# Performance work log

Hardware: AMD Instinct MI355X
Metric: run time of the kernel (lower is better)

Reference implementation:

```python
import jax, jax.numpy as jnp
import numpy as np

SCALE_FACTORS = (1, 2, 4)
N, T, F = 4096, 128, 128
MARKET = 64
MIX = sum(T // k for k in SCALE_FACTORS)  # 224


def hardswish(x):
    return x * jnp.clip(x + 3.0, 0.0, 6.0) * (1.0 / 6.0)


def layernorm2d(x, g, b, eps=1e-5):
    # LayerNorm with normalized_shape == last two dims (as in torch nn.LayerNorm((A, B)))
    mu = jnp.mean(x, axis=(-2, -1), keepdims=True)
    var = jnp.var(x, axis=(-2, -1), keepdims=True)
    return (x - mu) * jax.lax.rsqrt(var + eps) * g + b


def setup_inputs() -> dict:
    key = jax.random.key(0)
    ks = jax.random.split(key, 32)
    inp = {"x": jax.random.normal(ks[0], (N, T, F), jnp.float32)}
    i = 1
    for si, k in enumerate(SCALE_FACTORS):
        tk = T // k
        inp[f"cw{si}"] = jax.random.normal(ks[i], (F, F, k), jnp.float32) * 0.05; i += 1
        inp[f"cb{si}"] = jnp.zeros((F,), jnp.float32)
        inp[f"lg{si}"] = jnp.ones((tk, F), jnp.float32)
        inp[f"lb{si}"] = jnp.zeros((tk, F), jnp.float32)
        inp[f"L1_{si}"] = jax.random.normal(ks[i], (tk, tk), jnp.float32) * 0.01; i += 1
        inp[f"L2_{si}"] = jax.random.normal(ks[i], (tk, tk), jnp.float32) * 0.01; i += 1
    inp["fc_w"] = jax.random.normal(ks[i], (1, F), jnp.float32) * 0.05; i += 1
    inp["fc_b"] = jnp.zeros((1,), jnp.float32)
    inp["sm_lg"] = jnp.ones((N, MIX), jnp.float32)
    inp["sm_lb"] = jnp.zeros((N, MIX), jnp.float32)
    inp["M1"] = jax.random.normal(ks[i], (MARKET, N), jnp.float32); i += 1
    inp["M2"] = jax.random.normal(ks[i], (N, MARKET), jnp.float32); i += 1
    inp["sm_fc_w"] = jax.random.normal(ks[i], (1, 2 * MIX), jnp.float32) * 0.02; i += 1
    inp["sm_fc_b"] = jnp.zeros((1,), jnp.float32)
    return inp


def _forward(x, cw0, cb0, lg0, lb0, L1_0, L2_0,
             cw1, cb1, lg1, lb1, L1_1, L2_1,
             cw2, cb2, lg2, lb2, L1_2, L2_2,
             fc_w, fc_b, sm_lg, sm_lb, M1, M2, sm_fc_w, sm_fc_b):
    n, t, f = x.shape
    per_scale = ((cw0, cb0, lg0, lb0, L1_0, L2_0),
                 (cw1, cb1, lg1, lb1, L1_1, L2_1),
                 (cw2, cb2, lg2, lb2, L1_2, L2_2))
    parts = []
    for k, (cw, cb, lg, lb, L1, L2) in zip(SCALE_FACTORS, per_scale):
        tk = t // k
        # Conv1d(kernel=k, stride=k) == blockwise contraction over non-overlapping windows
        xr = x.transpose(0, 2, 1).reshape(n, f, tk, k)          # (n, F_in, tk, k)
        xt = jnp.einsum('nitk,oik->nto', xr, cw) + cb            # (n, tk, F)
        # TimeMixing: ragged prefix loop == single lower-triangular matmul over time
        mask = jnp.tril(jnp.ones((tk, tk), x.dtype))
        h = layernorm2d(xt, lg, lb)
        u = hardswish(jnp.einsum('ts,nsf->ntf', L1 * mask, h))
        v = jnp.einsum('ts,nsf->ntf', L2 * mask, u)
        xt = xt + v
        parts.append(xt @ fc_w[0] + fc_b[0])                     # (n, tk)
    h = jnp.concatenate(parts, axis=1)                           # (n, MIX)
    # StockMixing
    hn = layernorm2d(h, sm_lg, sm_lb)
    z = M2 @ hardswish(M1 @ hn)                                  # (n, MIX)
    out = jnp.concatenate([h, h + z], axis=1)                    # (n, 2*MIX)
    return out @ sm_fc_w[0][:, None] + sm_fc_b                   # (n, 1)


def reference(x, cw0, cb0, lg0, lb0, L1_0, L2_0,
              cw1, cb1, lg1, lb1, L1_1, L2_1,
              cw2, cb2, lg2, lb2, L1_2, L2_2,
              fc_w, fc_b, sm_lg, sm_lb, M1, M2, sm_fc_w, sm_fc_b):
    return _forward(x, cw0, cb0, lg0, lb0, L1_0, L2_0,
                    cw1, cb1, lg1, lb1, L1_1, L2_1,
                    cw2, cb2, lg2, lb2, L1_2, L2_2,
                    fc_w, fc_b, sm_lg, sm_lb, M1, M2, sm_fc_w, sm_fc_b)
```

## Files before the change

### kernel.cpp

```cpp
#include <hip/hip_runtime.h>
#include <stdint.h>

typedef __attribute__((ext_vector_type(8))) short short8;
typedef __attribute__((ext_vector_type(4))) float f32x4;
typedef __attribute__((ext_vector_type(4))) unsigned short us4;

__device__ __forceinline__ unsigned short f2bf(float f) {
  union { float f; unsigned int i; } v; v.f = f;
  return (unsigned short)((v.i + 0x7FFFu + ((v.i >> 16) & 1u)) >> 16);
}
__device__ __forceinline__ float hswish(float x) {
  float t = fminf(fmaxf(x + 3.f, 0.f), 6.f);
  return x * t * (1.f / 6.f);
}
__device__ __forceinline__ short8 ldcvt8(const float* __restrict__ p) {
  float4 v0 = *(const float4*)p;
  float4 v1 = *(const float4*)(p + 4);
  short8 r;
  r[0] = (short)f2bf(v0.x); r[1] = (short)f2bf(v0.y);
  r[2] = (short)f2bf(v0.z); r[3] = (short)f2bf(v0.w);
  r[4] = (short)f2bf(v1.x); r[5] = (short)f2bf(v1.y);
  r[6] = (short)f2bf(v1.z); r[7] = (short)f2bf(v1.w);
  return r;
}

#define WS16_OFF   0ULL
#define M1T_OFF    425984ULL
#define LGT0_OFF   1474560ULL
#define LBT0_OFF   1540096ULL
#define LGT1_OFF   1605632ULL
#define LBT1_OFF   1638400ULL
#define LGT2_OFF   1671168ULL
#define LBT2_OFF   1687552ULL
#define H_OFF      1703936ULL
#define HT_OFF     5373952ULL
#define STATS_OFF  9043968ULL
#define A_OFF      9044224ULL
#define CVEC_OFF   9101568ULL
#define XBF_OFF    9437184ULL
#define WS_NEED    143654912ULL

__global__ void prep_kernel(const float* __restrict__ cw0, const float* __restrict__ cw1,
                            const float* __restrict__ cw2,
                            const float* __restrict__ L1_0, const float* __restrict__ L2_0,
                            const float* __restrict__ L1_1, const float* __restrict__ L2_1,
                            const float* __restrict__ L1_2, const float* __restrict__ L2_2,
                            const float* __restrict__ M1,
                            const float* __restrict__ lg0, const float* __restrict__ lb0,
                            const float* __restrict__ lg1, const float* __restrict__ lb1,
                            const float* __restrict__ lg2, const float* __restrict__ lb2,
                            char* __restrict__ ws) {
  unsigned short* ws16 = (unsigned short*)(ws + WS16_OFF);
  float* m1t  = (float*)(ws + M1T_OFF);
  float* lgT0 = (float*)(ws + LGT0_OFF); float* lbT0 = (float*)(ws + LBT0_OFF);
  float* lgT1 = (float*)(ws + LGT1_OFF); float* lbT1 = (float*)(ws + LBT1_OFF);
  float* lgT2 = (float*)(ws + LGT2_OFF); float* lbT2 = (float*)(ws + LBT2_OFF);
  int idx = blockIdx.x * 256 + threadIdx.x;
  if (idx < 16384) {
    ws16[idx] = f2bf(cw0[idx]);
  } else if (idx < 49152) {
    int t = idx - 16384; int o = t >> 8, m = t & 255, j = m >> 7, i = m & 127;
    ws16[idx] = f2bf(cw1[(o * 128 + i) * 2 + j]);
  } else if (idx < 114688) {
    int t = idx - 49152; int o = t >> 9, m = t & 511, j = m >> 7, i = m & 127;
    ws16[idx] = f2bf(cw2[(o * 128 + i) * 4 + j]);
  } else if (idx < 212992) {
    int u = idx - 114688; int which = u >> 14; int e = u & 16383;
    int t = e >> 7, s = e & 127;
    float val = 0.f;
    if (which == 0)      { if (s <= t) val = L1_0[t * 128 + s]; }
    else if (which == 1) { if (s <= t) val = L2_0[t * 128 + s]; }
    else if (which == 2) { if ((s >> 6) == (t >> 6) && (s & 63) <= (t & 63)) val = L1_1[(t & 63) * 64 + (s & 63)]; }
    else if (which == 3) { if ((s >> 6) == (t >> 6) && (s & 63) <= (t & 63)) val = L2_1[(t & 63) * 64 + (s & 63)]; }
    else if (which == 4) { if ((s >> 5) == (t >> 5) && (s & 31) <= (t & 31)) val = L1_2[(t & 31) * 32 + (s & 31)]; }
    else                 { if ((s >> 5) == (t >> 5) && (s & 31) <= (t & 31)) val = L2_2[(t & 31) * 32 + (s & 31)]; }
    ws16[idx] = f2bf(val);
  } else if (idx < 475136) {
    int e = idx - 212992; int n = e >> 6, r = e & 63;
    m1t[e] = M1[r * 4096 + n];
  } else if (idx < 491520) {
    int e = idx - 475136; int f = e >> 7, t = e & 127; lgT0[e] = lg0[t * 128 + f];
  } else if (idx < 507904) {
    int e = idx - 491520; int f = e >> 7, t = e & 127; lbT0[e] = lb0[t * 128 + f];
  } else if (idx < 516096) {
    int e = idx - 507904; int f = e >> 6, t = e & 63;  lgT1[e] = lg1[t * 128 + f];
  } else if (idx < 524288) {
    int e = idx - 516096; int f = e >> 6, t = e & 63;  lbT1[e] = lb1[t * 128 + f];
  } else if (idx < 528384) {
    int e = idx - 524288; int f = e >> 5, t = e & 31;  lgT2[e] = lg2[t * 128 + f];
  } else if (idx < 532480) {
    int e = idx - 528384; int f = e >> 5, t = e & 31;  lbT2[e] = lb2[t * 128 + f];
  }
}

__global__ void xcvt_kernel(const float* __restrict__ x, unsigned short* __restrict__ xbf) {
  const float4* x4 = (const float4*)x;
  us4* o4 = (us4*)xbf;
#pragma unroll
  for (int j = 0; j < 4; ++j) {
    int idx = blockIdx.x * 1024 + j * 256 + threadIdx.x;
    float4 v = x4[idx];
    us4 p; p[0] = f2bf(v.x); p[1] = f2bf(v.y); p[2] = f2bf(v.z); p[3] = f2bf(v.w);
    o4[idx] = p;
  }
}

template <int S, bool XBF>
__device__ __forceinline__ void s1_body(
    int bidx,
    const float* __restrict__ xf, const unsigned short* __restrict__ xb,
    const float* __restrict__ cb, const float* __restrict__ lgT, const float* __restrict__ lbT,
    const float* __restrict__ fc_w, const float* __restrict__ fc_b,
    const unsigned short* __restrict__ cwLT,
    const unsigned short* __restrict__ L1blk, const unsigned short* __restrict__ L2blk,
    float* __restrict__ h_out, float* __restrict__ hT, float* __restrict__ stats,
    unsigned short* __restrict__ HT, float* __restrict__ scr) {
  constexpr int K = 128 << S;
  constexpr int LOG2TK = 7 - S;
  constexpr int TKM = (128 >> S) - 1;
  constexpr int TK = 128 >> S;
  constexpr int SAMPLES = 1 << S;
  constexpr int OFF = (S == 0) ? 0 : (S == 1 ? 128 : 192);
  constexpr int NK = K / 32;
  constexpr int GSH = 3 - S;
  constexpr float INVD = 1.f / (float)(TK * 128);

  float* part = scr + 128;
  const int tid = threadIdx.x, wave = tid >> 6, lane = tid & 63;
  const int quad = lane >> 4, l16 = lane & 15;
  const int Tb = (wave & 1) * 4, Ob = (wave >> 1) * 4;
  const int n0 = bidx << S;
  const size_t xbase = (size_t)n0 * 16384;

  if (tid < 128) { scr[tid] = fc_w[tid]; part[tid] = 0.f; }
  else if (tid < 144) scr[tid + 128] = 0.f;
  __syncthreads();

  f32x4 acc[4][4];
#pragma unroll
  for (int tt = 0; tt < 4; ++tt)
#pragma unroll
    for (int oo = 0; oo < 4; ++oo) acc[tt][oo] = (f32x4){0.f, 0.f, 0.f, 0.f};
#pragma unroll 4
  for (int ks = 0; ks < NK; ++ks) {
    short8 a[4];
#pragma unroll
    for (int tt = 0; tt < 4; ++tt) {
      size_t off = xbase + (size_t)((Tb + tt) * 16 + l16) * K + ks * 32 + quad * 8;
      if constexpr (XBF) a[tt] = *(const short8*)&xb[off];
      else a[tt] = ldcvt8(xf + off);
    }
#pragma unroll
    for (int oo = 0; oo < 4; ++oo) {
      short8 b = *(const short8*)&cwLT[((Ob + oo) * 16 + l16) * K + ks * 32 + quad * 8];
#pragma unroll
      for (int tt = 0; tt < 4; ++tt)
        acc[tt][oo] = __builtin_amdgcn_mfma_f32_16x16x32_bf16(a[tt], b, acc[tt][oo], 0, 0, 0);
    }
  }

  float ts[4] = {0.f, 0.f, 0.f, 0.f}, tq[4] = {0.f, 0.f, 0.f, 0.f};
#pragma unroll
  for (int oo = 0; oo < 4; ++oo) {
    float cbv = cb[(Ob + oo) * 16 + l16];
#pragma unroll
    for (int tt = 0; tt < 4; ++tt)
#pragma unroll
      for (int r = 0; r < 4; ++r) {
        float v = acc[tt][oo][r] + cbv;
        acc[tt][oo][r] = v;
        ts[tt] += v; tq[tt] += v * v;
      }
  }
  {
    constexpr int GPW = (S == 2) ? 2 : 1;
    float gs[2] = {0.f, 0.f}, gq[2] = {0.f, 0.f};
#pragma unroll
    for (int tt = 0; tt < 4; ++tt) {
      int gl = (S == 2) ? (tt >> 1) : 0;
      gs[gl] += ts[tt]; gq[gl] += tq[tt];
    }
#pragma unroll
    for (int j = 0; j < GPW; ++j) {
      float s = gs[j], q = gq[j];
#pragma unroll
      for (int m = 32; m >= 1; m >>= 1) { s += __shfl_xor(s, m); q += __shfl_xor(q, m); }
      if (lane == 0) {
        int g = (Tb >> GSH) + j;
        atomicAdd(&scr[256 + 2 * g], s);
        atomicAdd(&scr[257 + 2 * g], q);
      }
    }
  }
  __syncthreads();
  if (tid < SAMPLES) {
    float mu = scr[256 + 2 * tid] * INVD;
    float var = scr[257 + 2 * tid] * INVD - mu * mu;
    scr[264 + tid] = mu; scr[268 + tid] = rsqrtf(var + 1e-5f);
  }
  __syncthreads();

#pragma unroll
  for (int tt = 0; tt < 4; ++tt)
#pragma unroll
    for (int r = 0; r < 4; ++r) {
      float v = 0.f;
#pragma unroll
      for (int oo = 0; oo < 4; ++oo) v += acc[tt][oo][r] * scr[(Ob + oo) * 16 + l16];
      v += __shfl_xor(v, 1); v += __shfl_xor(v, 2);
      v += __shfl_xor(v, 4); v += __shfl_xor(v, 8);
      if (l16 == 0) atomicAdd(&part[(Tb + tt) * 16 + quad * 4 + r], v);
    }

#pragma unroll
  for (int tt = 0; tt < 4; ++tt) {
    int tile = Tb + tt, g = tile >> GSH;
    float mu = scr[264 + g], rs = scr[268 + g];
    int tb = tile * 16 + quad * 4;
    int tl = tb & TKM;
#pragma unroll
    for (int oo = 0; oo < 4; ++oo) {
      int f = (Ob + oo) * 16 + l16;
      int kf = (f ^ (f >> 3)) & 15;
      float4 lg4 = *(const float4*)&lgT[f * TK + tl];
      float4 lb4 = *(const float4*)&lbT[f * TK + tl];
#pragma unroll
      for (int r = 0; r < 4; ++r) {
        int t = tb + r;
        float hv = (acc[tt][oo][r] - mu) * rs * (&lg4.x)[r] + (&lb4.x)[r];
        HT[f * 128 + ((((t >> 3) ^ kf) << 3) | (t & 7))] = f2bf(hv);
      }
    }
  }
  __syncthreads();

  f32x4 u[4][4];
#pragma unroll
  for (int tt = 0; tt < 4; ++tt)
#pragma unroll
    for (int oo = 0; oo < 4; ++oo) u[tt][oo] = (f32x4){0.f, 0.f, 0.f, 0.f};
#pragma unroll
  for (int ks = 0; ks < 4; ++ks) {
    short8 a[4]; bool act[4]; bool any = false;
#pragma unroll
    for (int tt = 0; tt < 4; ++tt) {
      int tile = Tb + tt, g = tile >> GSH;
      act[tt] = (ks * 32 <= tile * 16 + 15) && (ks * 32 + 31 >= (g << LOG2TK));
      if (act[tt]) { a[tt] = *(const short8*)&L1blk[(tile * 16 + l16) * 128 + ks * 32 + quad * 8]; any = true; }
    }
    if (!any) continue;
#pragma unroll
    for (int oo = 0; oo < 4; ++oo) {
      int f = (Ob + oo) * 16 + l16;
      int kf = (f ^ (f >> 3)) & 15;
      short8 b = *(const short8*)&HT[f * 128 + (((ks * 4 + quad) ^ kf) << 3)];
#pragma unroll
      for (int tt = 0; tt < 4; ++tt)
        if (act[tt]) u[tt][oo] = __builtin_amdgcn_mfma_f32_16x16x32_bf16(a[tt], b, u[tt][oo], 0, 0, 0);
    }
  }
  __syncthreads();

#pragma unroll
  for (int tt = 0; tt < 4; ++tt) {
    int tile = Tb + tt;
    int tb = tile * 16 + quad * 4;
#pragma unroll
    for (int oo = 0; oo < 4; ++oo) {
      int f = (Ob + oo) * 16 + l16;
      int kf = (f ^ (f >> 3)) & 15;
#pragma unroll
      for (int r = 0; r < 4; ++r) {
        int t = tb + r;
        HT[f * 128 + ((((t >> 3) ^ kf) << 3) | (t & 7))] = f2bf(hswish(u[tt][oo][r]));
      }
    }
  }
  __syncthreads();

#pragma unroll
  for (int tt = 0; tt < 4; ++tt)
#pragma unroll
    for (int oo = 0; oo < 4; ++oo) u[tt][oo] = (f32x4){0.f, 0.f, 0.f, 0.f};
#pragma unroll
  for (int ks = 0; ks < 4; ++ks) {
    short8 a[4]; bool act[4]; bool any = false;
#pragma unroll
    for (int tt = 0; tt < 4; ++tt) {
      int tile = Tb + tt, g = tile >> GSH;
      act[tt] = (ks * 32 <= tile * 16 + 15) && (ks * 32 + 31 >= (g << LOG2TK));
      if (act[tt]) { a[tt] = *(const short8*)&L2blk[(tile * 16 + l16) * 128 + ks * 32 + quad * 8]; any = true; }
    }
    if (!any) continue;
#pragma unroll
    for (int oo = 0; oo < 4; ++oo) {
      int f = (Ob + oo) * 16 + l16;
      int kf = (f ^ (f >> 3)) & 15;
      short8 b = *(const short8*)&HT[f * 128 + (((ks * 4 + quad) ^ kf) << 3)];
#pragma unroll
      for (int tt = 0; tt < 4; ++tt)
        if (act[tt]) u[tt][oo] = __builtin_amdgcn_mfma_f32_16x16x32_bf16(a[tt], b, u[tt][oo], 0, 0, 0);
    }
  }

#pragma unroll
  for (int tt = 0; tt < 4; ++tt)
#pragma unroll
    for (int r = 0; r < 4; ++r) {
      float v = 0.f;
#pragma unroll
      for (int oo = 0; oo < 4; ++oo) v += u[tt][oo][r] * scr[(Ob + oo) * 16 + l16];
      v += __shfl_xor(v, 1); v += __shfl_xor(v, 2);
      v += __shfl_xor(v, 4); v += __shfl_xor(v, 8);
      if (l16 == 0) atomicAdd(&part[(Tb + tt) * 16 + quad * 4 + r], v);
    }
  __syncthreads();

  if (tid < 128) {
    float val = part[tid] + fc_b[0];
    int g = tid >> LOG2TK, tl = tid & TKM;
    int n = n0 + g;
    h_out[(size_t)n * 224 + OFF + tl] = val;
    hT[(size_t)(OFF + tl) * 4096 + n] = val;
    float s = val, q = val * val;
#pragma unroll
    for (int m = 32; m >= 1; m >>= 1) { s += __shfl_xor(s, m); q += __shfl_xor(q, m); }
    if (lane == 0) {
      int slot = (int)(blockIdx.x & 31);
      atomicAdd(&stats[2 * slot], s);
      atomicAdd(&stats[2 * slot + 1], q);
    }
  }
}

template <bool XBF>
__launch_bounds__(256, 4)
__global__ void s1_all(const float* __restrict__ xf, const unsigned short* __restrict__ xb,
                       const float* __restrict__ cb0, const float* __restrict__ cb1,
                       const float* __restrict__ cb2,
                       const float* __restrict__ fc_w, const float* __restrict__ fc_b,
                       const char* __restrict__ wsc,
                       float* __restrict__ h_out, float* __restrict__ hT,
                       float* __restrict__ stats) {
  __shared__ unsigned short HT[128 * 128];
  __shared__ float scr[272];
  const unsigned short* ws16 = (const unsigned short*)(wsc + WS16_OFF);
  int b = blockIdx.x;
  if (b < 1024) {
    s1_body<2, XBF>(b, xf, xb, cb2,
                    (const float*)(wsc + LGT2_OFF), (const float*)(wsc + LBT2_OFF),
                    fc_w, fc_b, ws16 + 49152, ws16 + 180224, ws16 + 196608,
                    h_out, hT, stats, HT, scr);
  } else if (b < 3072) {
    s1_body<1, XBF>(b - 1024, xf, xb, cb1,
                    (const float*)(wsc + LGT1_OFF), (const float*)(wsc + LBT1_OFF),
                    fc_w, fc_b, ws16 + 16384, ws16 + 147456, ws16 + 163840,
                    h_out, hT, stats, HT, scr);
  } else {
    s1_body<0, XBF>(b - 3072, xf, xb, cb0,
                    (const float*)(wsc + LGT0_OFF), (const float*)(wsc + LBT0_OFF),
                    fc_w, fc_b, ws16, ws16 + 114688, ws16 + 131072,
                    h_out, hT, stats, HT, scr);
  }
}

__global__ void mix1_kernel(const float* __restrict__ hT,
                            const float* __restrict__ sm_lg,
                            const float* __restrict__ sm_lb,
                            const float* __restrict__ m1t,
                            const float* __restrict__ stats,
                            float* __restrict__ A) {
  const int m = blockIdx.x;
  const int seg = blockIdx.y;
  const int r = threadIdx.x & 63, c = threadIdx.x >> 6;
  float S = 0.f, Q = 0.f;
#pragma unroll
  for (int s = 0; s < 32; ++s) { S += stats[2 * s]; Q += stats[2 * s + 1]; }
  const float inv = 1.f / 917504.f;
  float mu = S * inv;
  float rsig = rsqrtf(Q * inv - mu * mu + 1e-5f);
  float acc = 0.f;
  const int n0 = seg * 512 + c * 128;
  for (int i = 0; i < 128; ++i) {
    int n = n0 + i;
    float hn = (hT[m * 4096 + n] - mu) * rsig * sm_lg[n * 224 + m] + sm_lb[n * 224 + m];
    acc += m1t[n * 64 + r] * hn;
  }
  __shared__ float red[256];
  red[threadIdx.x] = acc;
  __syncthreads();
  if (threadIdx.x < 64)
    atomicAdd(&A[threadIdx.x * 224 + m],
              red[threadIdx.x] + red[64 + threadIdx.x] + red[128 + threadIdx.x] + red[192 + threadIdx.x]);
}

__global__ void mix2_kernel(const float* __restrict__ A,
                            const float* __restrict__ sm_fc_w,
                            float* __restrict__ cvec) {
  int r = threadIdx.x & 63, ch = threadIdx.x >> 6;
  float acc = 0.f;
  for (int j = ch; j < 224; j += 4)
    acc += hswish(A[r * 224 + j]) * sm_fc_w[224 + j];
  __shared__ float red[256];
  red[threadIdx.x] = acc;
  __syncthreads();
  if (threadIdx.x < 64)
    cvec[threadIdx.x] = red[threadIdx.x] + red[64 + threadIdx.x] + red[128 + threadIdx.x] + red[192 + threadIdx.x];
}

__global__ void out_kernel(const float* __restrict__ h,
                           const float* __restrict__ M2,
                           const float* __restrict__ cvec,
                           const float* __restrict__ sm_fc_w,
                           const float* __restrict__ sm_fc_b,
                           float* __restrict__ out) {
  int wave = threadIdx.x >> 6, lane = threadIdx.x & 63;
  int n = blockIdx.x * 4 + wave;
  float acc = M2[n * 64 + lane] * cvec[lane];
  for (int j = lane; j < 224; j += 64)
    acc += h[n * 224 + j] * (sm_fc_w[j] + sm_fc_w[224 + j]);
#pragma unroll
  for (int m = 32; m >= 1; m >>= 1) acc += __shfl_xor(acc, m);
  if (lane == 0) out[n] = acc + sm_fc_b[0];
}

extern "C" void kernel_launch(void* const* d_in, const int* in_sizes, int n_in,
                              void* d_out, int out_size, void* d_ws, size_t ws_size,
                              hipStream_t stream) {
  const float* x      = (const float*)d_in[0];
  const float* cw0    = (const float*)d_in[1];
  const float* cb0    = (const float*)d_in[2];
  const float* lg0    = (const float*)d_in[3];
  const float* lb0    = (const float*)d_in[4];
  const float* L1_0   = (const float*)d_in[5];
  const float* L2_0   = (const float*)d_in[6];
  const float* cw1    = (const float*)d_in[7];
  const float* cb1    = (const float*)d_in[8];
  const float* lg1    = (const float*)d_in[9];
  const float* lb1    = (const float*)d_in[10];
  const float* L1_1   = (const float*)d_in[11];
  const float* L2_1   = (const float*)d_in[12];
  const float* cw2    = (const float*)d_in[13];
  const float* cb2    = (const float*)d_in[14];
  const float* lg2    = (const float*)d_in[15];
  const float* lb2    = (const float*)d_in[16];
  const float* L1_2   = (const float*)d_in[17];
  const float* L2_2   = (const float*)d_in[18];
  const float* fc_w   = (const float*)d_in[19];
  const float* fc_b   = (const float*)d_in[20];
  const float* sm_lg  = (const float*)d_in[21];
  const float* sm_lb  = (const float*)d_in[22];
  const float* M1     = (const float*)d_in[23];
  const float* M2     = (const float*)d_in[24];
  const float* sm_fc_w = (const float*)d_in[25];
  const float* sm_fc_b = (const float*)d_in[26];

  char* ws = (char*)d_ws;
  float* m1t   = (float*)(ws + M1T_OFF);
  float* h     = (float*)(ws + H_OFF);
  float* hT    = (float*)(ws + HT_OFF);
  float* stats = (float*)(ws + STATS_OFF);
  float* A     = (float*)(ws + A_OFF);
  float* cvec  = (float*)(ws + CVEC_OFF);
  unsigned short* xbf = (unsigned short*)(ws + XBF_OFF);
  const bool use_xbf = ws_size >= WS_NEED;

  prep_kernel<<<2080, 256, 0, stream>>>(cw0, cw1, cw2, L1_0, L2_0, L1_1, L2_1, L1_2, L2_2,
                                        M1, lg0, lb0, lg1, lb1, lg2, lb2, ws);
  hipMemsetAsync(ws + STATS_OFF, 0, 256 + 57344, stream);

  if (use_xbf) {
    xcvt_kernel<<<16384, 256, 0, stream>>>(x, xbf);
    s1_all<true><<<7168, 256, 0, stream>>>(x, xbf, cb0, cb1, cb2, fc_w, fc_b, ws, h, hT, stats);
  } else {
    s1_all<false><<<7168, 256, 0, stream>>>(x, xbf, cb0, cb1, cb2, fc_w, fc_b, ws, h, hT, stats);
  }

  mix1_kernel<<<dim3(224, 8), 256, 0, stream>>>(hT, sm_lg, sm_lb, m1t, stats, A);
  mix2_kernel<<<1, 256, 0, stream>>>(A, sm_fc_w, cvec);
  out_kernel<<<1024, 256, 0, stream>>>(h, M2, cvec, sm_fc_w, sm_fc_b, (float*)d_out);
}
```

Before: 999.1 us.

## Split fused multi-scale kernel into per-scale launches and drop transposed h buffer

Replaces the single branching s1_all kernel with three templated per-scale launches, each with launch bounds of 3 waves-per-SIMD instead of 4, and removes the unroll pragma on the K loop. The transposed hT copy is no longer written; mix1 now reads h directly with strided access and uses fewer, longer segments. Each per-scale kernel can get its own register allocation instead of the worst case across scales, at the cost of extra launches, lost overlap between scales, and less coalesced reads in mix1.

```diff
diff --git a/kernel.cpp b/kernel.cpp
--- a/kernel.cpp
+++ b/kernel.cpp
@@ -33,12 +33,11 @@
 #define LGT2_OFF   1671168ULL
 #define LBT2_OFF   1687552ULL
 #define H_OFF      1703936ULL
-#define HT_OFF     5373952ULL
-#define STATS_OFF  9043968ULL
-#define A_OFF      9044224ULL
-#define CVEC_OFF   9101568ULL
-#define XBF_OFF    9437184ULL
-#define WS_NEED    143654912ULL
+#define STATS_OFF  5373952ULL
+#define A_OFF      5374208ULL
+#define CVEC_OFF   5431552ULL
+#define XBF_OFF    8388608ULL
+#define WS_NEED    142606336ULL
 
 __global__ void prep_kernel(const float* __restrict__ cw0, const float* __restrict__ cw1,
                             const float* __restrict__ cw2,
@@ -106,15 +105,15 @@
 }
 
 template <int S, bool XBF>
-__device__ __forceinline__ void s1_body(
-    int bidx,
-    const float* __restrict__ xf, const unsigned short* __restrict__ xb,
-    const float* __restrict__ cb, const float* __restrict__ lgT, const float* __restrict__ lbT,
-    const float* __restrict__ fc_w, const float* __restrict__ fc_b,
-    const unsigned short* __restrict__ cwLT,
-    const unsigned short* __restrict__ L1blk, const unsigned short* __restrict__ L2blk,
-    float* __restrict__ h_out, float* __restrict__ hT, float* __restrict__ stats,
-    unsigned short* __restrict__ HT, float* __restrict__ scr) {
+__launch_bounds__(256, 3)
+__global__ void s1_tile(const float* __restrict__ xf, const unsigned short* __restrict__ xb,
+                        const float* __restrict__ cb,
+                        const float* __restrict__ lgT, const float* __restrict__ lbT,
+                        const float* __restrict__ fc_w, const float* __restrict__ fc_b,
+                        const unsigned short* __restrict__ cwLT,
+                        const unsigned short* __restrict__ L1blk,
+                        const unsigned short* __restrict__ L2blk,
+                        float* __restrict__ h_out, float* __restrict__ stats) {
   constexpr int K = 128 << S;
   constexpr int LOG2TK = 7 - S;
   constexpr int TKM = (128 >> S) - 1;
@@ -125,11 +124,14 @@
   constexpr int GSH = 3 - S;
   constexpr float INVD = 1.f / (float)(TK * 128);
 
+  __shared__ unsigned short HT[128 * 128];
+  __shared__ float scr[272];
   float* part = scr + 128;
+
   const int tid = threadIdx.x, wave = tid >> 6, lane = tid & 63;
   const int quad = lane >> 4, l16 = lane & 15;
   const int Tb = (wave & 1) * 4, Ob = (wave >> 1) * 4;
-  const int n0 = bidx << S;
+  const int n0 = blockIdx.x << S;
   const size_t xbase = (size_t)n0 * 16384;
 
   if (tid < 128) { scr[tid] = fc_w[tid]; part[tid] = 0.f; }
@@ -141,7 +143,6 @@
   for (int tt = 0; tt < 4; ++tt)
 #pragma unroll
     for (int oo = 0; oo < 4; ++oo) acc[tt][oo] = (f32x4){0.f, 0.f, 0.f, 0.f};
-#pragma unroll 4
   for (int ks = 0; ks < NK; ++ks) {
     short8 a[4];
 #pragma unroll
@@ -319,9 +320,7 @@
   if (tid < 128) {
     float val = part[tid] + fc_b[0];
     int g = tid >> LOG2TK, tl = tid & TKM;
-    int n = n0 + g;
-    h_out[(size_t)n * 224 + OFF + tl] = val;
-    hT[(size_t)(OFF + tl) * 4096 + n] = val;
+    h_out[(size_t)(n0 + g) * 224 + OFF + tl] = val;
     float s = val, q = val * val;
 #pragma unroll
     for (int m = 32; m >= 1; m >>= 1) { s += __shfl_xor(s, m); q += __shfl_xor(q, m); }
@@ -333,38 +332,7 @@
   }
 }
 
-template <bool XBF>
-__launch_bounds__(256, 4)
-__global__ void s1_all(const float* __restrict__ xf, const unsigned short* __restrict__ xb,
-                       const float* __restrict__ cb0, const float* __restrict__ cb1,
-                       const float* __restrict__ cb2,
-                       const float* __restrict__ fc_w, const float* __restrict__ fc_b,
-                       const char* __restrict__ wsc,
-                       float* __restrict__ h_out, float* __restrict__ hT,
-                       float* __restrict__ stats) {
-  __shared__ unsigned short HT[128 * 128];
-  __shared__ float scr[272];
-  const unsigned short* ws16 = (const unsigned short*)(wsc + WS16_OFF);
-  int b = blockIdx.x;
-  if (b < 1024) {
-    s1_body<2, XBF>(b, xf, xb, cb2,
-                    (const float*)(wsc + LGT2_OFF), (const float*)(wsc + LBT2_OFF),
-                    fc_w, fc_b, ws16 + 49152, ws16 + 180224, ws16 + 196608,
-                    h_out, hT, stats, HT, scr);
-  } else if (b < 3072) {
-    s1_body<1, XBF>(b - 1024, xf, xb, cb1,
-                    (const float*)(wsc + LGT1_OFF), (const float*)(wsc + LBT1_OFF),
-                    fc_w, fc_b, ws16 + 16384, ws16 + 147456, ws16 + 163840,
-                    h_out, hT, stats, HT, scr);
-  } else {
-    s1_body<0, XBF>(b - 3072, xf, xb, cb0,
-                    (const float*)(wsc + LGT0_OFF), (const float*)(wsc + LBT0_OFF),
-                    fc_w, fc_b, ws16, ws16 + 114688, ws16 + 131072,
-                    h_out, hT, stats, HT, scr);
-  }
-}
-
-__global__ void mix1_kernel(const float* __restrict__ hT,
+__global__ void mix1_kernel(const float* __restrict__ h,
                             const float* __restrict__ sm_lg,
                             const float* __restrict__ sm_lb,
                             const float* __restrict__ m1t,
@@ -380,10 +348,10 @@
   float mu = S * inv;
   float rsig = rsqrtf(Q * inv - mu * mu + 1e-5f);
   float acc = 0.f;
-  const int n0 = seg * 512 + c * 128;
-  for (int i = 0; i < 128; ++i) {
+  const int n0 = seg * 1024 + c * 256;
+  for (int i = 0; i < 256; ++i) {
     int n = n0 + i;
-    float hn = (hT[m * 4096 + n] - mu) * rsig * sm_lg[n * 224 + m] + sm_lb[n * 224 + m];
+    float hn = (h[n * 224 + m] - mu) * rsig * sm_lg[n * 224 + m] + sm_lb[n * 224 + m];
     acc += m1t[n * 64 + r] * hn;
   }
   __shared__ float red[256];
@@ -456,27 +424,47 @@
   const float* sm_fc_b = (const float*)d_in[26];
 
   char* ws = (char*)d_ws;
+  unsigned short* ws16 = (unsigned short*)(ws + WS16_OFF);
   float* m1t   = (float*)(ws + M1T_OFF);
   float* h     = (float*)(ws + H_OFF);
-  float* hT    = (float*)(ws + HT_OFF);
   float* stats = (float*)(ws + STATS_OFF);
   float* A     = (float*)(ws + A_OFF);
   float* cvec  = (float*)(ws + CVEC_OFF);
   unsigned short* xbf = (unsigned short*)(ws + XBF_OFF);
   const bool use_xbf = ws_size >= WS_NEED;
 
+  const unsigned short* cwLT0 = ws16;
+  const unsigned short* cwLT1 = ws16 + 16384;
+  const unsigned short* cwLT2 = ws16 + 49152;
+  const unsigned short* L1b0 = ws16 + 114688;
+  const unsigned short* L2b0 = ws16 + 131072;
+  const unsigned short* L1b1 = ws16 + 147456;
+  const unsigned short* L2b1 = ws16 + 163840;
+  const unsigned short* L1b2 = ws16 + 180224;
+  const unsigned short* L2b2 = ws16 + 196608;
+  const float* lgT0 = (const float*)(ws + LGT0_OFF);
+  const float* lbT0 = (const float*)(ws + LBT0_OFF);
+  const float* lgT1 = (const float*)(ws + LGT1_OFF);
+  const float* lbT1 = (const float*)(ws + LBT1_OFF);
+  const float* lgT2 = (const float*)(ws + LGT2_OFF);
+  const float* lbT2 = (const float*)(ws + LBT2_OFF);
+
   prep_kernel<<<2080, 256, 0, stream>>>(cw0, cw1, cw2, L1_0, L2_0, L1_1, L2_1, L1_2, L2_2,
                                         M1, lg0, lb0, lg1, lb1, lg2, lb2, ws);
   hipMemsetAsync(ws + STATS_OFF, 0, 256 + 57344, stream);
 
   if (use_xbf) {
     xcvt_kernel<<<16384, 256, 0, stream>>>(x, xbf);
-    s1_all<true><<<7168, 256, 0, stream>>>(x, xbf, cb0, cb1, cb2, fc_w, fc_b, ws, h, hT, stats);
+    s1_tile<0, true><<<4096, 256, 0, stream>>>(x, xbf, cb0, lgT0, lbT0, fc_w, fc_b, cwLT0, L1b0, L2b0, h, stats);
+    s1_tile<1, true><<<2048, 256, 0, stream>>>(x, xbf, cb1, lgT1, lbT1, fc_w, fc_b, cwLT1, L1b1, L2b1, h, stats);
+    s1_tile<2, true><<<1024, 256, 0, stream>>>(x, xbf, cb2, lgT2, lbT2, fc_w, fc_b, cwLT2, L1b2, L2b2, h, stats);
   } else {
-    s1_all<false><<<7168, 256, 0, stream>>>(x, xbf, cb0, cb1, cb2, fc_w, fc_b, ws, h, hT, stats);
-  }
-
-  mix1_kernel<<<dim3(224, 8), 256, 0, stream>>>(hT, sm_lg, sm_lb, m1t, stats, A);
+    s1_tile<0, false><<<4096, 256, 0, stream>>>(x, xbf, cb0, lgT0, lbT0, fc_w, fc_b, cwLT0, L1b0, L2b0, h, stats);
+    s1_tile<1, false><<<2048, 256, 0, stream>>>(x, xbf, cb1, lgT1, lbT1, fc_w, fc_b, cwLT1, L1b1, L2b1, h, stats);
+    s1_tile<2, false><<<1024, 256, 0, stream>>>(x, xbf, cb2, lgT2, lbT2, fc_w, fc_b, cwLT2, L1b2, L2b2, h, stats);
+  }
+
+  mix1_kernel<<<dim3(224, 4), 256, 0, stream>>>(h, sm_lg, sm_lb, m1t, stats, A);
   mix2_kernel<<<1, 256, 0, stream>>>(A, sm_fc_w, cvec);
   out_kernel<<<1024, 256, 0, stream>>>(h, M2, cvec, sm_fc_w, sm_fc_b, (float*)d_out);
 }
```

New measurement: 951.8 us. 1.05x faster.
